# Optimization experiments

Hardware: AMD Instinct MI355X
Metric: run time of the kernel (lower is better)

Reference implementation:

```python
import jax, jax.numpy as jnp
import numpy as np

D_MODEL = 1024
HEADS = 16
D_K = D_MODEL // HEADS
NEG_INF = -1e10


def setup_inputs() -> dict:
    key = jax.random.key(0)
    ks = jax.random.split(key, 10)
    n, s = 2, 2048
    inp = {
        "value": jax.random.normal(ks[0], (n, s, D_MODEL), dtype=jnp.float32),
        "key": jax.random.normal(ks[1], (n, s, D_MODEL), dtype=jnp.float32),
        "query": jax.random.normal(ks[2], (n, s, D_MODEL), dtype=jnp.float32),
        "mask": jax.random.randint(ks[3], (n, 1, s, s), 0, 2, dtype=jnp.int32),
        # torch.nn.Linear weights are [out, in]; y = x @ W.T (+ b)
        "Wq": jax.random.normal(ks[4], (D_MODEL, D_MODEL), dtype=jnp.float32) * (D_MODEL ** -0.5),
        "Wk": jax.random.normal(ks[5], (D_MODEL, D_MODEL), dtype=jnp.float32) * (D_MODEL ** -0.5),
        "Wv": jax.random.normal(ks[6], (D_MODEL, D_MODEL), dtype=jnp.float32) * (D_MODEL ** -0.5),
        "Wo": jax.random.normal(ks[7], (D_MODEL, D_MODEL), dtype=jnp.float32) * (D_MODEL ** -0.5),
        "bo": jax.random.normal(ks[8], (D_MODEL,), dtype=jnp.float32) * 0.01,
    }
    return inp


def reference(value, key, query, mask, Wq, Wk, Wv, Wo, bo):
    n, q_len, _ = query.shape
    # projections (Linear, no bias): x @ W.T
    q = (query @ Wq.T).reshape(n, q_len, HEADS, D_K)
    k = (key @ Wk.T).reshape(n, key.shape[1], HEADS, D_K)
    v = (value @ Wv.T).reshape(n, value.shape[1], HEADS, D_K)
    scores = jnp.einsum('nqhd,nkhd->nhqk', q, k)  # [n,h,q,k]
    scores = jnp.where(mask == 0, jnp.float32(NEG_INF), scores)
    attn = jax.nn.softmax(scores / jnp.sqrt(jnp.float32(D_K)), axis=-1)
    out = jnp.einsum('nhql,nlhd->nqhd', attn, v).reshape(n, q_len, D_MODEL)
    return out @ Wo.T + bo
```

## Files before the change

### kernel.cpp

```cpp
#include <hip/hip_runtime.h>
#include <hip/hip_bf16.h>
#include <stdint.h>

#define SEQ     2048
#define NBATCH  2
#define DMODEL  1024
#define NH      16
#define DKH     64

typedef __bf16 bf16;
typedef __attribute__((ext_vector_type(8))) __bf16 bf16x8;
typedef __attribute__((ext_vector_type(4))) __bf16 bf16x4;
typedef __attribute__((ext_vector_type(4))) float  f32x4;

static __device__ __forceinline__ f32x4 mfma16(bf16x8 a, bf16x8 b, f32x4 c) {
    return __builtin_amdgcn_mfma_f32_16x16x32_bf16(a, b, c, 0, 0, 0);
}

typedef const __attribute__((address_space(1))) void* gas_cptr;
typedef __attribute__((address_space(3))) void*       las_ptr;
#define GLDS16(g, l) __builtin_amdgcn_global_load_lds((gas_cptr)(g), (las_ptr)(l), 16, 0, 0)

__global__ __launch_bounds__(256) void cvt_all_k(const float* __restrict__ q,
                                                 const float* __restrict__ k,
                                                 const float* __restrict__ v,
                                                 const float* __restrict__ wq,
                                                 const float* __restrict__ wk,
                                                 const float* __restrict__ wv,
                                                 const float* __restrict__ wo,
                                                 bf16* __restrict__ qb, bf16* __restrict__ kb,
                                                 bf16* __restrict__ vb, bf16* __restrict__ wqb,
                                                 bf16* __restrict__ wkb, bf16* __restrict__ wvb,
                                                 bf16* __restrict__ wob) {
    const float* src; bf16* dst; int n4;
    const int NX4 = (NBATCH * SEQ * DMODEL) / 4, NW4 = (DMODEL * DMODEL) / 4;
    switch (blockIdx.y) {
        case 0: src = q;  dst = qb;  n4 = NX4; break;
        case 1: src = k;  dst = kb;  n4 = NX4; break;
        case 2: src = v;  dst = vb;  n4 = NX4; break;
        case 3: src = wq; dst = wqb; n4 = NW4; break;
        case 4: src = wk; dst = wkb; n4 = NW4; break;
        case 5: src = wv; dst = wvb; n4 = NW4; break;
        default: src = wo; dst = wob; n4 = NW4; break;
    }
    int stride = gridDim.x * blockDim.x;
    for (int i = blockIdx.x * blockDim.x + threadIdx.x; i < n4; i += stride) {
        f32x4 f = ((const f32x4*)src)[i];
        bf16x4 o;
#pragma unroll
        for (int j = 0; j < 4; j++) o[j] = (bf16)f[j];
        ((bf16x4*)dst)[i] = o;
    }
}

__global__ __launch_bounds__(256) void pack_mask_k(const int* __restrict__ mask,
                                                   unsigned long long* __restrict__ bits,
                                                   int nwords) {
    int wave  = (blockIdx.x * blockDim.x + threadIdx.x) >> 6;
    int lane  = threadIdx.x & 63;
    int nwtot = (gridDim.x * blockDim.x) >> 6;
    for (int w = wave; w < nwords; w += nwtot) {
        int m = mask[(size_t)w * 64 + lane];
        unsigned long long b = __ballot(m != 0);
        if (lane == 0) bits[w] = b;
    }
}

__global__ __launch_bounds__(256) void qkv_gemm(const bf16* __restrict__ Xq,
                                                const bf16* __restrict__ Xk,
                                                const bf16* __restrict__ Xv,
                                                const bf16* __restrict__ Wq,
                                                const bf16* __restrict__ Wk,
                                                const bf16* __restrict__ Wv,
                                                bf16* __restrict__ Qo,
                                                bf16* __restrict__ Ko,
                                                bf16* __restrict__ Vto) {
    __shared__ bf16 As[128 * 32], Bs[128 * 32];
    const int z = blockIdx.z;
    const bf16* A = (z == 0) ? Xq : (z == 1) ? Xk : Xv;
    const bf16* W = (z == 0) ? Wq : (z == 1) ? Wk : Wv;
    const int bm = blockIdx.x * 128, bn = blockIdx.y * 128;
    const int tid = threadIdx.x, wave = tid >> 6, lane = tid & 63;
    const int wm = wave >> 1, wn = wave & 1, lo = lane & 15, hi = lane >> 4;

    const int r0 = wave * 32 + (lane >> 2);
    const int c8 = (lane & 3) * 8;
    const bf16* Ag = A + (size_t)(bm + r0) * DMODEL + c8;
    const bf16* Bg = W + (size_t)(bn + r0) * DMODEL + c8;
    bf16* lA = &As[wave * 1024];
    bf16* lB = &Bs[wave * 1024];

    f32x4 acc[4][4];
#pragma unroll
    for (int i = 0; i < 4; i++)
#pragma unroll
        for (int j = 0; j < 4; j++) acc[i][j] = 0.0f;

    for (int k0 = 0; k0 < DMODEL; k0 += 32) {
        __syncthreads();
        GLDS16(Ag + k0, lA);
        GLDS16(Ag + k0 + (size_t)16 * DMODEL, lA + 512);
        GLDS16(Bg + k0, lB);
        GLDS16(Bg + k0 + (size_t)16 * DMODEL, lB + 512);
        __syncthreads();

        bf16x8 a[4], b[4];
#pragma unroll
        for (int t = 0; t < 4; t++) {
            a[t] = *(const bf16x8*)&As[(wm * 64 + t * 16 + lo) * 32 + hi * 8];
            b[t] = *(const bf16x8*)&Bs[(wn * 64 + t * 16 + lo) * 32 + hi * 8];
        }
#pragma unroll
        for (int tm = 0; tm < 4; tm++)
#pragma unroll
            for (int tn = 0; tn < 4; tn++)
                acc[tm][tn] = mfma16(a[tm], b[tn], acc[tm][tn]);
    }

    if (z < 2) {
        bf16* O = (z == 0) ? Qo : Ko;
#pragma unroll
        for (int tm = 0; tm < 4; tm++)
#pragma unroll
            for (int tn = 0; tn < 4; tn++)
#pragma unroll
                for (int r = 0; r < 4; r++) {
                    int m = bm + wm * 64 + tm * 16 + hi * 4 + r;
                    int o = bn + wn * 64 + tn * 16 + lo;
                    int nidx = m >> 11, sq = m & 2047;
                    int hh = o >> 6, d = o & 63;
                    O[(((size_t)nidx * NH + hh) * SEQ + sq) * DKH + d] = (bf16)acc[tm][tn][r];
                }
    } else {
#pragma unroll
        for (int tm = 0; tm < 4; tm++)
#pragma unroll
            for (int tn = 0; tn < 4; tn++)
#pragma unroll
                for (int r = 0; r < 4; r++) {
                    int m = bm + wm * 64 + tm * 16 + hi * 4 + r;
                    int o = bn + wn * 64 + tn * 16 + lo;
                    int nidx = m >> 11, sq = m & 2047;
                    int hh = o >> 6, d = o & 63;
                    Vto[(((size_t)nidx * NH + hh) * DKH + d) * SEQ + sq] = (bf16)acc[tm][tn][r];
                }
    }
}

__global__ __launch_bounds__(256, 5) void attn_k(const bf16* __restrict__ Q,
                                                 const bf16* __restrict__ K,
                                                 const bf16* __restrict__ Vt,
                                                 const unsigned long long* __restrict__ mbits,
                                                 bf16* __restrict__ Op0,
                                                 bf16* __restrict__ Op1,
                                                 float* __restrict__ Lp) {
    __shared__ bf16 Ks[64 * 72];
    __shared__ bf16 Vs[64 * 72];
    __shared__ bf16 Ps[64 * 72];

    const int bid = blockIdx.x;
    const int xcd = bid & 7, j = bid >> 3;
    const int hd = xcd * 4 + (j & 3);
    const int qb = (j >> 2) & 31;
    const int ks = j >> 7;
    const int n = hd >> 4, h = hd & 15;

    const int tid = threadIdx.x, wave = tid >> 6, lane = tid & 63;
    const int lo = lane & 15, hi = lane >> 4;

    const size_t headoff = (size_t)hd * SEQ * DKH;
    const bf16* Qh = Q + headoff;
    const bf16* Kh = K + headoff;
    const bf16* Vh = Vt + headoff;

    const int qrow = qb * 64 + wave * 16 + lo;
    const bf16x8 aq0 = *(const bf16x8*)(Qh + (size_t)qrow * DKH + hi * 8);
    const bf16x8 aq1 = *(const bf16x8*)(Qh + (size_t)qrow * DKH + 32 + hi * 8);

    bf16x8 ones;
#pragma unroll
    for (int i = 0; i < 8; i++) ones[i] = (bf16)1.0f;

    f32x4 oacc[4];
#pragma unroll
    for (int t = 0; t < 4; t++) oacc[t] = 0.0f;
    f32x4 lacc; lacc = 0.0f;

    const unsigned long long* mb = mbits + ((size_t)n * SEQ + qb * 64 + wave * 16) * (SEQ / 64);
    const float c = 0.18033688f;

    const int kbeg = ks * 1024, kend = kbeg + 1024;

    const int srow = tid >> 3, sseg = tid & 7;
    const bf16* Kg = Kh + (size_t)srow * DKH + sseg * 8;
    const bf16* Vg = Vh + (size_t)srow * SEQ + sseg * 8;

    bf16x8 rk0 = *(const bf16x8*)(Kg + (size_t)kbeg * DKH);
    bf16x8 rk1 = *(const bf16x8*)(Kg + (size_t)(kbeg + 32) * DKH);
    bf16x8 rv0 = *(const bf16x8*)(Vg + kbeg);
    bf16x8 rv1 = *(const bf16x8*)(Vg + (size_t)32 * SEQ + kbeg);

    for (int k0 = kbeg; k0 < kend; k0 += 64) {
        __syncthreads();
        *(bf16x8*)&Ks[srow * 72 + sseg * 8]        = rk0;
        *(bf16x8*)&Ks[(srow + 32) * 72 + sseg * 8] = rk1;
        *(bf16x8*)&Vs[srow * 72 + sseg * 8]        = rv0;
        *(bf16x8*)&Vs[(srow + 32) * 72 + sseg * 8] = rv1;
        if (k0 + 64 < kend) {
            rk0 = *(const bf16x8*)(Kg + (size_t)(k0 + 64) * DKH);
            rk1 = *(const bf16x8*)(Kg + (size_t)(k0 + 96) * DKH);
            rv0 = *(const bf16x8*)(Vg + k0 + 64);
            rv1 = *(const bf16x8*)(Vg + (size_t)32 * SEQ + k0 + 64);
        }
        __syncthreads();

        unsigned long long w64[4];
#pragma unroll
        for (int r = 0; r < 4; r++) w64[r] = mb[(size_t)(hi * 4 + r) * (SEQ / 64) + (k0 >> 6)];

        f32x4 s[4];
#pragma unroll
        for (int tn = 0; tn < 4; tn++) {
            const int kr = (tn * 16 + lo) * 72;
            bf16x8 b0 = *(const bf16x8*)&Ks[kr + hi * 8];
            bf16x8 b1 = *(const bf16x8*)&Ks[kr + 32 + hi * 8];
            f32x4 z4; z4 = 0.0f;
            z4 = mfma16(aq0, b0, z4);
            z4 = mfma16(aq1, b1, z4);
            s[tn] = z4;
        }

#pragma unroll
        for (int r = 0; r < 4; r++) {
            unsigned wlo = (unsigned)(w64[r] >> lo);
            unsigned whi = (unsigned)(w64[r] >> (lo + 32));
#pragma unroll
            for (int tn = 0; tn < 4; tn++) {
                unsigned bit = ((tn < 2 ? wlo : whi) >> ((tn & 1) * 16)) & 1u;
                float pv = exp2f(s[tn][r] * c);
                pv = bit ? pv : 0.0f;
                Ps[(wave * 16 + hi * 4 + r) * 72 + tn * 16 + lo] = (bf16)pv;
            }
        }
        asm volatile("s_waitcnt lgkmcnt(0)" ::: "memory");

        bf16x8 ap0 = *(const bf16x8*)&Ps[(wave * 16 + lo) * 72 + hi * 8];
        bf16x8 ap1 = *(const bf16x8*)&Ps[(wave * 16 + lo) * 72 + 32 + hi * 8];
#pragma unroll
        for (int td = 0; td < 4; td++) {
            bf16x8 b0 = *(const bf16x8*)&Vs[(td * 16 + lo) * 72 + hi * 8];
            bf16x8 b1 = *(const bf16x8*)&Vs[(td * 16 + lo) * 72 + 32 + hi * 8];
            oacc[td] = mfma16(ap0, b0, oacc[td]);
            oacc[td] = mfma16(ap1, b1, oacc[td]);
        }
        lacc = mfma16(ap0, ones, lacc);
        lacc = mfma16(ap1, ones, lacc);
    }

    bf16* Op = ks ? Op1 : Op0;
#pragma unroll
    for (int td = 0; td < 4; td++)
#pragma unroll
        for (int r = 0; r < 4; r++) {
            int q = qb * 64 + wave * 16 + hi * 4 + r;
            int d = td * 16 + lo;
            Op[((size_t)n * SEQ + q) * DMODEL + h * 64 + d] = (bf16)oacc[td][r];
        }
    if (lo == 0) {
#pragma unroll
        for (int r = 0; r < 4; r++) {
            int q = qb * 64 + wave * 16 + hi * 4 + r;
            Lp[(size_t)ks * (NBATCH * NH * SEQ) + ((size_t)(n * NH + h) * SEQ) + q] = lacc[r];
        }
    }
}

__global__ __launch_bounds__(256) void merge_k(const bf16* __restrict__ o0,
                                               const bf16* __restrict__ o1,
                                               const float* __restrict__ lp,
                                               bf16* __restrict__ Aout) {
    int t = blockIdx.x * blockDim.x + threadIdx.x;
    int q = t >> 7;
    int h = (t >> 3) & 15;
    int n = q >> 11;
    bf16x8 a = ((const bf16x8*)o0)[t];
    bf16x8 b = ((const bf16x8*)o1)[t];
    int li = (n * NH + h) * SEQ + (q & 2047);
    float l = lp[li] + lp[NBATCH * NH * SEQ + li];
    float rl = 1.0f / l;
    bf16x8 o;
#pragma unroll
    for (int i = 0; i < 8; i++) o[i] = (bf16)(((float)a[i] + (float)b[i]) * rl);
    ((bf16x8*)Aout)[t] = o;
}

__global__ __launch_bounds__(256) void out_gemm(const bf16* __restrict__ A,
                                                const bf16* __restrict__ W,
                                                const float* __restrict__ bias,
                                                float* __restrict__ Out) {
    __shared__ bf16 As[128 * 32], Bs[128 * 32];
    const int bm = blockIdx.x * 128, bn = blockIdx.y * 128;
    const int tid = threadIdx.x, wave = tid >> 6, lane = tid & 63;
    const int wm = wave >> 1, wn = wave & 1, lo = lane & 15, hi = lane >> 4;

    const int r0 = wave * 32 + (lane >> 2);
    const int c8 = (lane & 3) * 8;
    const bf16* Ag = A + (size_t)(bm + r0) * DMODEL + c8;
    const bf16* Bg = W + (size_t)(bn + r0) * DMODEL + c8;
    bf16* lA = &As[wave * 1024];
    bf16* lB = &Bs[wave * 1024];

    f32x4 acc[4][4];
#pragma unroll
    for (int i = 0; i < 4; i++)
#pragma unroll
        for (int j = 0; j < 4; j++) acc[i][j] = 0.0f;

    for (int k0 = 0; k0 < DMODEL; k0 += 32) {
        __syncthreads();
        GLDS16(Ag + k0, lA);
        GLDS16(Ag + k0 + (size_t)16 * DMODEL, lA + 512);
        GLDS16(Bg + k0, lB);
        GLDS16(Bg + k0 + (size_t)16 * DMODEL, lB + 512);
        __syncthreads();

        bf16x8 a[4], b[4];
#pragma unroll
        for (int t = 0; t < 4; t++) {
            a[t] = *(const bf16x8*)&As[(wm * 64 + t * 16 + lo) * 32 + hi * 8];
            b[t] = *(const bf16x8*)&Bs[(wn * 64 + t * 16 + lo) * 32 + hi * 8];
        }
#pragma unroll
        for (int tm = 0; tm < 4; tm++)
#pragma unroll
            for (int tn = 0; tn < 4; tn++)
                acc[tm][tn] = mfma16(a[tm], b[tn], acc[tm][tn]);
    }

#pragma unroll
    for (int tm = 0; tm < 4; tm++)
#pragma unroll
        for (int tn = 0; tn < 4; tn++) {
            int o = bn + wn * 64 + tn * 16 + lo;
            float bv = bias[o];
#pragma unroll
            for (int r = 0; r < 4; r++) {
                int m = bm + wm * 64 + tm * 16 + hi * 4 + r;
                Out[(size_t)m * DMODEL + o] = acc[tm][tn][r] + bv;
            }
        }
}

extern "C" void kernel_launch(void* const* d_in, const int* in_sizes, int n_in,
                              void* d_out, int out_size, void* d_ws, size_t ws_size,
                              hipStream_t stream) {
    const float* value = (const float*)d_in[0];
    const float* key   = (const float*)d_in[1];
    const float* query = (const float*)d_in[2];
    const int*   mask  = (const int*)d_in[3];
    const float* Wq    = (const float*)d_in[4];
    const float* Wk    = (const float*)d_in[5];
    const float* Wv    = (const float*)d_in[6];
    const float* Wo    = (const float*)d_in[7];
    const float* bo    = (const float*)d_in[8];
    float* out = (float*)d_out;

    char* ws = (char*)d_ws;
    bf16* Qws = (bf16*)(ws);
    bf16* Kws = (bf16*)(ws + (8u  << 20));
    bf16* Vt  = (bf16*)(ws + (16u << 20));
    bf16* Xqb = (bf16*)(ws + (24u << 20));
    bf16* Xkb = (bf16*)(ws + (32u << 20));
    bf16* Xvb = (bf16*)(ws + (40u << 20));
    bf16* Wqb = (bf16*)(ws + (48u << 20));
    bf16* Wkb = (bf16*)(ws + (50u << 20));
    bf16* Wvb = (bf16*)(ws + (52u << 20));
    bf16* Wob = (bf16*)(ws + (54u << 20));
    unsigned long long* mbits = (unsigned long long*)(ws + (56u << 20));
    bf16*  Op0 = Xqb;
    bf16*  Op1 = Xkb;
    bf16*  Aws = Xvb;
    float* Lp  = (float*)Wqb;

    cvt_all_k<<<dim3(1024, 7), 256, 0, stream>>>(query, key, value, Wq, Wk, Wv, Wo,
                                                 Xqb, Xkb, Xvb, Wqb, Wkb, Wvb, Wob);
    pack_mask_k<<<1024, 256, 0, stream>>>(mask, mbits, NBATCH * SEQ * (SEQ / 64));
    qkv_gemm<<<dim3(32, 8, 3), 256, 0, stream>>>(Xqb, Xkb, Xvb, Wqb, Wkb, Wvb, Qws, Kws, Vt);
    attn_k<<<2048, 256, 0, stream>>>(Qws, Kws, Vt, mbits, Op0, Op1, Lp);
    merge_k<<<2048, 256, 0, stream>>>(Op0, Op1, Lp, Aws);
    out_gemm<<<dim3(32, 8), 256, 0, stream>>>(Aws, Wob, bo, out);
}
```

Before: 301.7 us.

## Keep attention probabilities in registers via permlane swaps instead of LDS round-trip

Computes S transposed (K as the A operand) so each lane holds a column of probabilities, packs them to bf16 with v_cvt_pk_bf16_f32, and rearranges them with v_permlane32/16 swaps into the A-operand layout for the PV MFMA. This removes the Ps shared-memory buffer along with its store, wait and reload. The softmax scale is folded into the Q projection epilogue, the raw exp2 builtin replaces exp2f, and the mask is read as a single 64-bit word per row with prefetch. Occupancy is raised from 5 to 6 blocks per SIMD. The risks are the correctness of the lane permutation and added register pressure.

```diff
diff --git a/kernel.cpp b/kernel.cpp
--- a/kernel.cpp
+++ b/kernel.cpp
@@ -20,6 +20,9 @@
 typedef const __attribute__((address_space(1))) void* gas_cptr;
 typedef __attribute__((address_space(3))) void*       las_ptr;
 #define GLDS16(g, l) __builtin_amdgcn_global_load_lds((gas_cptr)(g), (las_ptr)(l), 16, 0, 0)
+
+#define PL32SWAP(a, b) asm("v_permlane32_swap_b32 %0, %1" : "+v"(a), "+v"(b))
+#define PL16SWAP(a, b) asm("v_permlane16_swap_b32 %0, %1" : "+v"(a), "+v"(b))
 
 __global__ __launch_bounds__(256) void cvt_all_k(const float* __restrict__ q,
                                                  const float* __restrict__ k,
@@ -119,6 +122,7 @@
 
     if (z < 2) {
         bf16* O = (z == 0) ? Qo : Ko;
+        const float qscale = (z == 0) ? 0.18033688f : 1.0f;
 #pragma unroll
         for (int tm = 0; tm < 4; tm++)
 #pragma unroll
@@ -129,7 +133,7 @@
                     int o = bn + wn * 64 + tn * 16 + lo;
                     int nidx = m >> 11, sq = m & 2047;
                     int hh = o >> 6, d = o & 63;
-                    O[(((size_t)nidx * NH + hh) * SEQ + sq) * DKH + d] = (bf16)acc[tm][tn][r];
+                    O[(((size_t)nidx * NH + hh) * SEQ + sq) * DKH + d] = (bf16)(acc[tm][tn][r] * qscale);
                 }
     } else {
 #pragma unroll
@@ -147,7 +151,7 @@
     }
 }
 
-__global__ __launch_bounds__(256, 5) void attn_k(const bf16* __restrict__ Q,
+__global__ __launch_bounds__(256, 6) void attn_k(const bf16* __restrict__ Q,
                                                  const bf16* __restrict__ K,
                                                  const bf16* __restrict__ Vt,
                                                  const unsigned long long* __restrict__ mbits,
@@ -156,7 +160,6 @@
                                                  float* __restrict__ Lp) {
     __shared__ bf16 Ks[64 * 72];
     __shared__ bf16 Vs[64 * 72];
-    __shared__ bf16 Ps[64 * 72];
 
     const int bid = blockIdx.x;
     const int xcd = bid & 7, j = bid >> 3;
@@ -186,8 +189,7 @@
     for (int t = 0; t < 4; t++) oacc[t] = 0.0f;
     f32x4 lacc; lacc = 0.0f;
 
-    const unsigned long long* mb = mbits + ((size_t)n * SEQ + qb * 64 + wave * 16) * (SEQ / 64);
-    const float c = 0.18033688f;
+    const unsigned long long* mbq = mbits + ((size_t)n * SEQ + qrow) * (SEQ / 64);
 
     const int kbeg = ks * 1024, kend = kbeg + 1024;
 
@@ -199,7 +201,10 @@
     bf16x8 rk1 = *(const bf16x8*)(Kg + (size_t)(kbeg + 32) * DKH);
     bf16x8 rv0 = *(const bf16x8*)(Vg + kbeg);
     bf16x8 rv1 = *(const bf16x8*)(Vg + (size_t)32 * SEQ + kbeg);
-
+    unsigned long long wm = mbq[kbeg >> 6];
+    unsigned long long wmn = 0;
+
+#pragma unroll 1
     for (int k0 = kbeg; k0 < kend; k0 += 64) {
         __syncthreads();
         *(bf16x8*)&Ks[srow * 72 + sseg * 8]        = rk0;
@@ -211,41 +216,49 @@
             rk1 = *(const bf16x8*)(Kg + (size_t)(k0 + 96) * DKH);
             rv0 = *(const bf16x8*)(Vg + k0 + 64);
             rv1 = *(const bf16x8*)(Vg + (size_t)32 * SEQ + k0 + 64);
-        }
-        __syncthreads();
-
-        unsigned long long w64[4];
-#pragma unroll
-        for (int r = 0; r < 4; r++) w64[r] = mb[(size_t)(hi * 4 + r) * (SEQ / 64) + (k0 >> 6)];
-
-        f32x4 s[4];
+            wmn = mbq[(k0 >> 6) + 1];
+        }
+        __syncthreads();
+
+        unsigned wlo = (unsigned)(wm >> (hi * 4));
+        unsigned whi = (unsigned)(wm >> (hi * 4 + 32));
+        uint32_t pk[4][2];
 #pragma unroll
         for (int tn = 0; tn < 4; tn++) {
             const int kr = (tn * 16 + lo) * 72;
             bf16x8 b0 = *(const bf16x8*)&Ks[kr + hi * 8];
             bf16x8 b1 = *(const bf16x8*)&Ks[kr + 32 + hi * 8];
             f32x4 z4; z4 = 0.0f;
-            z4 = mfma16(aq0, b0, z4);
-            z4 = mfma16(aq1, b1, z4);
-            s[tn] = z4;
-        }
-
-#pragma unroll
-        for (int r = 0; r < 4; r++) {
-            unsigned wlo = (unsigned)(w64[r] >> lo);
-            unsigned whi = (unsigned)(w64[r] >> (lo + 32));
-#pragma unroll
-            for (int tn = 0; tn < 4; tn++) {
-                unsigned bit = ((tn < 2 ? wlo : whi) >> ((tn & 1) * 16)) & 1u;
-                float pv = exp2f(s[tn][r] * c);
-                pv = bit ? pv : 0.0f;
-                Ps[(wave * 16 + hi * 4 + r) * 72 + tn * 16 + lo] = (bf16)pv;
+            z4 = mfma16(b0, aq0, z4);
+            z4 = mfma16(b1, aq1, z4);
+            unsigned ws = ((tn < 2) ? wlo : whi) >> ((tn & 1) * 16);
+            float pv[4];
+#pragma unroll
+            for (int r = 0; r < 4; r++) {
+                float e = __builtin_amdgcn_exp2f(z4[r]);
+                pv[r] = ((ws >> r) & 1u) ? e : 0.0f;
             }
-        }
-        asm volatile("s_waitcnt lgkmcnt(0)" ::: "memory");
-
-        bf16x8 ap0 = *(const bf16x8*)&Ps[(wave * 16 + lo) * 72 + hi * 8];
-        bf16x8 ap1 = *(const bf16x8*)&Ps[(wave * 16 + lo) * 72 + 32 + hi * 8];
+            asm("v_cvt_pk_bf16_f32 %0, %1, %2" : "=v"(pk[tn][0]) : "v"(pv[0]), "v"(pv[1]));
+            asm("v_cvt_pk_bf16_f32 %0, %1, %2" : "=v"(pk[tn][1]) : "v"(pv[2]), "v"(pv[3]));
+        }
+        wm = wmn;
+
+        uint32_t d00 = pk[0][0], d02 = pk[1][0];
+        PL32SWAP(d00, d02); PL16SWAP(d00, d02);
+        uint32_t d01 = pk[0][1], d03 = pk[1][1];
+        PL32SWAP(d01, d03); PL16SWAP(d01, d03);
+        uint32_t d10 = pk[2][0], d12 = pk[3][0];
+        PL32SWAP(d10, d12); PL16SWAP(d10, d12);
+        uint32_t d11 = pk[2][1], d13 = pk[3][1];
+        PL32SWAP(d11, d13); PL16SWAP(d11, d13);
+
+        union FragU { uint32_t u[4]; bf16x8 v; };
+        FragU f0, f1;
+        f0.u[0] = d00; f0.u[1] = d01; f0.u[2] = d02; f0.u[3] = d03;
+        f1.u[0] = d10; f1.u[1] = d11; f1.u[2] = d12; f1.u[3] = d13;
+        bf16x8 ap0 = f0.v;
+        bf16x8 ap1 = f1.v;
+
 #pragma unroll
         for (int td = 0; td < 4; td++) {
             bf16x8 b0 = *(const bf16x8*)&Vs[(td * 16 + lo) * 72 + hi * 8];
```

Result: faster. 281.0 us (-6.9%).
